# Performance work log

Measured on AMD Instinct MI355X. Metric: run time of the kernel, lower is better.

## Reference

```python
import jax, jax.numpy as jnp
import numpy as np

N_EMBD = 384
N_HEAD = 6
BLOCK_SIZE = 256


def setup_inputs() -> dict:
    key = jax.random.key(0)
    ks = jax.random.split(key, 5)
    B, T = 128, 256
    x = jax.random.normal(ks[0], (B, T, N_EMBD), dtype=jnp.float32)
    # torch nn.Linear weights are (out_features, in_features)
    w_attn = jax.random.normal(ks[1], (3 * N_EMBD, N_EMBD), dtype=jnp.float32) * (1.0 / np.sqrt(N_EMBD))
    b_attn = jax.random.normal(ks[2], (3 * N_EMBD,), dtype=jnp.float32) * 0.02
    w_proj = jax.random.normal(ks[3], (N_EMBD, N_EMBD), dtype=jnp.float32) * (1.0 / np.sqrt(N_EMBD))
    b_proj = jax.random.normal(ks[4], (N_EMBD,), dtype=jnp.float32) * 0.02
    return {"x": x, "w_attn": w_attn, "b_attn": b_attn, "w_proj": w_proj, "b_proj": b_proj}


def reference(x, w_attn, b_attn, w_proj, b_proj):
    B, T, C = x.shape
    hd = C // N_HEAD  # head dim = 64
    qkv = x @ w_attn.T + b_attn                      # [B,T,3C]
    q, k, v = jnp.split(qkv, 3, axis=2)
    # [B,T,C] -> [B,H,T,hd]
    q = q.reshape(B, T, N_HEAD, hd).transpose(0, 2, 1, 3)
    k = k.reshape(B, T, N_HEAD, hd).transpose(0, 2, 1, 3)
    v = v.reshape(B, T, N_HEAD, hd).transpose(0, 2, 1, 3)
    att = jnp.einsum("bhqd,bhkd->bhqk", q, k) * (1.0 / np.sqrt(hd))
    causal = jnp.tril(jnp.ones((T, T), dtype=bool))
    att = jnp.where(causal, att, -jnp.inf)
    att = jax.nn.softmax(att, axis=-1)
    y = jnp.einsum("bhqk,bhkd->bhqd", att, v)        # [B,H,T,hd]
    y = y.transpose(0, 2, 1, 3).reshape(B, T, C)
    return y @ w_proj.T + b_proj
```

## Files before the change

### kernel.cpp

```cpp
#include <hip/hip_runtime.h>
#include <stdint.h>


typedef unsigned short u16;
typedef __attribute__((ext_vector_type(8))) short short8;
typedef __attribute__((ext_vector_type(4))) short short4v;
typedef __attribute__((ext_vector_type(4))) float float4v;

__device__ __forceinline__ u16 f2b(float f){
  union { float f; uint32_t u; } cv; cv.f = f;
  uint32_t u = cv.u;
  u += 0x7FFFu + ((u >> 16) & 1u);
  return (u16)(u >> 16);
}

__device__ __forceinline__ float4v mfma16(short8 a, short8 b, float4v c){
  return __builtin_amdgcn_mfma_f32_16x16x32_bf16(a, b, c, 0, 0, 0);
}

__device__ __forceinline__ void gld16(const void* g, void* l){
  __builtin_amdgcn_global_load_lds((__attribute__((address_space(1))) const void*)g,
                                   (__attribute__((address_space(3))) void*)l, 16, 0, 0);
}

__global__ __launch_bounds__(256) void cvt3(
    const float* __restrict__ a, u16* __restrict__ da, int na,
    const float* __restrict__ b, u16* __restrict__ db, int nb,
    const float* __restrict__ c, u16* __restrict__ dc, int nc)
{
  const int total = na + nb + nc;
  for (int i = blockIdx.x * blockDim.x + threadIdx.x; i < total;
       i += gridDim.x * blockDim.x){
    const float* s; u16* d; int j = i;
    if (j < na)           { s = a; d = da; }
    else if (j < na + nb) { j -= na; s = b; d = db; }
    else                  { j -= na + nb; s = c; d = dc; }
    const float4 v = ((const float4*)s)[j];
    ushort4 o;
    o.x = f2b(v.x); o.y = f2b(v.y); o.z = f2b(v.z); o.w = f2b(v.w);
    ((ushort4*)d)[j] = o;
  }
}

template<bool OUT_BF16>
__global__ __launch_bounds__(256) void gemm_k(
    const u16* __restrict__ A, const u16* __restrict__ B,
    const float* __restrict__ bias, void* __restrict__ Cout,
    const int M, const int N, const int K)
{
  __shared__ u16 Alds[128*32];
  __shared__ u16 Blds[128*32];
  const int tid  = threadIdx.x;
  const int lane = tid & 63;
  const int wave = tid >> 6;
  const int lrow = lane & 15;
  const int g    = lane >> 4;
  const int tm = blockIdx.x * 128;
  const int tn = blockIdx.y * 128;
  const int wm = (wave >> 1) * 64;
  const int wn = (wave & 1) * 64;

  float4v acc[4][4];
  #pragma unroll
  for (int i = 0; i < 4; ++i)
    #pragma unroll
    for (int j = 0; j < 4; ++j) acc[i][j] = (float4v){0.f, 0.f, 0.f, 0.f};

  const int srow = lane >> 2;
  const int scol = (lane & 3) * 8;
  const int nkt = K >> 5;
  for (int kt = 0; kt < nkt; ++kt){
    #pragma unroll
    for (int j2 = 0; j2 < 2; ++j2){
      const int c = wave * 2 + j2;
      const int row = c * 16 + srow;
      gld16(A + (size_t)(tm + row) * K + kt * 32 + scol, &Alds[c * 512]);
      gld16(B + (size_t)(tn + row) * K + kt * 32 + scol, &Blds[c * 512]);
    }
    __syncthreads();
    short8 af[4], bfm[4];
    #pragma unroll
    for (int i = 0; i < 4; ++i){
      af[i]  = *(const short8*)&Alds[(wm + i * 16 + lrow) * 32 + g * 8];
      bfm[i] = *(const short8*)&Blds[(wn + i * 16 + lrow) * 32 + g * 8];
    }
    #pragma unroll
    for (int mi = 0; mi < 4; ++mi)
      #pragma unroll
      for (int ni = 0; ni < 4; ++ni)
        acc[mi][ni] = mfma16(af[mi], bfm[ni], acc[mi][ni]);
    __syncthreads();
  }

  #pragma unroll
  for (int mi = 0; mi < 4; ++mi){
    #pragma unroll
    for (int ni = 0; ni < 4; ++ni){
      const int gcol = tn + wn + ni * 16 + lrow;
      const float bs = bias[gcol];
      #pragma unroll
      for (int r = 0; r < 4; ++r){
        const int grow = tm + wm + mi * 16 + g * 4 + r;
        const float v = acc[mi][ni][r] + bs;
        if (OUT_BF16) ((u16*)Cout)[(size_t)grow * N + gcol] = f2b(v);
        else          ((float*)Cout)[(size_t)grow * N + gcol] = v;
      }
    }
  }
}

__global__ __launch_bounds__(256) void attn_k(
    const u16* __restrict__ qkv, u16* __restrict__ y)
{
  __shared__ u16 Klds[256 * 64];
  __shared__ u16 Vt[64 * 256];
  const int tid  = threadIdx.x;
  const int lane = tid & 63;
  const int wave = tid >> 6;
  const int lrow = lane & 15;
  const int g    = lane >> 4;
  const int bh = blockIdx.x;
  const int b = bh / 6, h = bh % 6;
  const u16* qb = qkv + (size_t)b * 256 * 1152 + h * 64;
  const u16* kb = qb + 384;
  const u16* vb = qb + 768;

  #pragma unroll
  for (int j = 0; j < 8; ++j){
    const int c = wave * 8 + j;
    const int row = c * 8 + (lane >> 3);
    const int col = (((lane & 7) ^ (lane >> 3)) << 3);
    gld16(kb + (size_t)row * 1152 + col, &Klds[c * 512]);
  }
  {
    const int d  = lane;
    const int t0 = wave * 64;
    const int sv = d & 15;
    #pragma unroll
    for (int c4 = 0; c4 < 16; ++c4){
      const size_t base = (size_t)(t0 + c4 * 4) * 1152 + d;
      const u16 e0 = vb[base];
      const u16 e1 = vb[base + 1152];
      const u16 e2 = vb[base + 2304];
      const u16 e3 = vb[base + 3456];
      short4v g4; g4[0] = (short)e0; g4[1] = (short)e1; g4[2] = (short)e2; g4[3] = (short)e3;
      const int pos = (t0 >> 2) + (c4 ^ sv);
      *(short4v*)&Vt[(size_t)d * 256 + (pos << 2)] = g4;
    }
  }
  __syncthreads();

  for (int it = 0; it < 4; ++it){
    const int rb = wave + it * 4;
    const int q0 = rb * 16;
    const u16* qrow = qb + (size_t)(q0 + lrow) * 1152 + g * 8;
    const short8 qf0 = *(const short8*)(qrow);
    const short8 qf1 = *(const short8*)(qrow + 32);

    float4v s[16];
    #pragma unroll
    for (int nt = 0; nt < 16; ++nt){
      if (nt <= rb){
        const int row = nt * 16 + lrow;
        const int sw = lrow & 7;
        const short8 k0 = *(const short8*)&Klds[row * 64 + ((g ^ sw) << 3)];
        const short8 k1 = *(const short8*)&Klds[row * 64 + (((4 + g) ^ sw) << 3)];
        float4v a = (float4v){0.f, 0.f, 0.f, 0.f};
        a = mfma16(k0, qf0, a);
        a = mfma16(k1, qf1, a);
        if (nt == rb){
          #pragma unroll
          for (int r = 0; r < 4; ++r)
            a[r] = (g * 4 + r > lrow) ? -1e30f : a[r];
        }
        s[nt] = a;
      }
    }

    float mx = -1e30f;
    #pragma unroll
    for (int nt = 0; nt < 16; ++nt) if (nt <= rb){
      #pragma unroll
      for (int r = 0; r < 4; ++r) mx = fmaxf(mx, s[nt][r]);
    }
    mx = fmaxf(mx, __shfl_xor(mx, 16));
    mx = fmaxf(mx, __shfl_xor(mx, 32));
    float sum = 0.f;
    #pragma unroll
    for (int nt = 0; nt < 16; ++nt) if (nt <= rb){
      #pragma unroll
      for (int r = 0; r < 4; ++r){
        const float p = exp2f((s[nt][r] - mx) * 0.18033688011112042f);
        s[nt][r] = p;
        sum += p;
      }
    }
    sum += __shfl_xor(sum, 16);
    sum += __shfl_xor(sum, 32);
    const float rs = 1.f / sum;
    #pragma unroll
    for (int nt = 0; nt < 16; ++nt) if (nt <= rb) s[nt] *= rs;

    float4v o0 = (float4v){0,0,0,0}, o1 = (float4v){0,0,0,0};
    float4v o2 = (float4v){0,0,0,0}, o3 = (float4v){0,0,0,0};
    const int svr = lrow;
    #pragma unroll
    for (int kt = 0; kt < 8; ++kt){
      if (2 * kt <= rb){
        short8 pa;
        #pragma unroll
        for (int r = 0; r < 4; ++r) pa[r] = (short)f2b(s[2 * kt][r]);
        if (2 * kt + 1 <= rb){
          #pragma unroll
          for (int r = 0; r < 4; ++r) pa[4 + r] = (short)f2b(s[2 * kt + 1][r]);
        } else {
          #pragma unroll
          for (int r = 0; r < 4; ++r) pa[4 + r] = 0;
        }
        const int plo = ((kt * 8 + g) ^ svr) << 2;
        const int phi = ((kt * 8 + 4 + g) ^ svr) << 2;
        #pragma unroll
        for (int dt = 0; dt < 4; ++dt){
          const u16* vrow = &Vt[(size_t)(dt * 16 + lrow) * 256];
          const short4v vlo = *(const short4v*)&vrow[plo];
          const short4v vhi = *(const short4v*)&vrow[phi];
          const short8 bf = __builtin_shufflevector(vlo, vhi, 0,1,2,3,4,5,6,7);
          if      (dt == 0) o0 = mfma16(pa, bf, o0);
          else if (dt == 1) o1 = mfma16(pa, bf, o1);
          else if (dt == 2) o2 = mfma16(pa, bf, o2);
          else              o3 = mfma16(pa, bf, o3);
        }
      }
    }

    u16* yb = y + (size_t)(b * 256 + q0) * 384 + h * 64;
    #pragma unroll
    for (int r = 0; r < 4; ++r){
      const int q = g * 4 + r;
      yb[(size_t)q * 384 +  0 + lrow] = f2b(o0[r]);
      yb[(size_t)q * 384 + 16 + lrow] = f2b(o1[r]);
      yb[(size_t)q * 384 + 32 + lrow] = f2b(o2[r]);
      yb[(size_t)q * 384 + 48 + lrow] = f2b(o3[r]);
    }
  }
}

extern "C" void kernel_launch(void* const* d_in, const int* in_sizes, int n_in,
                              void* d_out, int out_size, void* d_ws, size_t ws_size,
                              hipStream_t stream)
{
  const float* x      = (const float*)d_in[0];
  const float* w_attn = (const float*)d_in[1];
  const float* b_attn = (const float*)d_in[2];
  const float* w_proj = (const float*)d_in[3];
  const float* b_proj = (const float*)d_in[4];
  float* out = (float*)d_out;

  char* ws = (char*)d_ws;
  u16* xb  = (u16*)(ws);
  u16* wab = (u16*)(ws + 25165824);
  u16* wpb = (u16*)(ws + 26050560);
  u16* qkv = (u16*)(ws + 26345472);
  u16* yb  = (u16*)(ws + 101842944);
  if (ws_size < 127008768) return;

  cvt3<<<2048, 256, 0, stream>>>(x, xb, 3145728,
                                 w_attn, wab, 110592,
                                 w_proj, wpb, 36864);
  gemm_k<true ><<<dim3(256, 9), 256, 0, stream>>>(xb, wab, b_attn, qkv, 32768, 1152, 384);
  attn_k<<<768, 256, 0, stream>>>(qkv, yb);
  gemm_k<false><<<dim3(256, 3), 256, 0, stream>>>(yb, wpb, b_proj, out, 32768, 384, 384);
}
```

Baseline: 127.8 us.

## Double-buffer GEMM LDS tiles, XOR-swizzle LDS layout, and remap blocks per XCD

The GEMM kernel now keeps two LDS buffers and prefetches the next K-slice with global_load_lds while the current one feeds the MFMAs. This removes one barrier per iteration and overlaps loads with compute. The LDS column chunks are XOR-swizzled on both the store and load side to reduce bank conflicts. The launch becomes a 1D grid whose block IDs are remapped so each group of 8 consecutive IDs spreads contiguous M tiles across XCDs, aiming for better L2 reuse. The cost is double the LDS footprint, which may lower occupancy.

New measurement: 125.7 us. Within noise of the previous version (-1.6%).

```diff
diff --git a/kernel.cpp b/kernel.cpp
--- a/kernel.cpp
+++ b/kernel.cpp
@@ -48,15 +48,20 @@
     const float* __restrict__ bias, void* __restrict__ Cout,
     const int M, const int N, const int K)
 {
-  __shared__ u16 Alds[128*32];
-  __shared__ u16 Blds[128*32];
+  __shared__ u16 Alds[2][128*32];
+  __shared__ u16 Blds[2][128*32];
   const int tid  = threadIdx.x;
   const int lane = tid & 63;
   const int wave = tid >> 6;
   const int lrow = lane & 15;
   const int g    = lane >> 4;
-  const int tm = blockIdx.x * 128;
-  const int tn = blockIdx.y * 128;
+
+  const int id    = blockIdx.x;
+  const int local = id >> 3;
+  const int xt = (id & 7) * 32 + (local & 31);
+  const int yt = local >> 5;
+  const int tm = xt * 128;
+  const int tn = yt * 128;
   const int wm = (wave >> 1) * 64;
   const int wn = (wave & 1) * 64;
 
@@ -67,22 +72,30 @@
     for (int j = 0; j < 4; ++j) acc[i][j] = (float4v){0.f, 0.f, 0.f, 0.f};
 
   const int srow = lane >> 2;
-  const int scol = (lane & 3) * 8;
+  const int sg   = ((lane & 3) ^ ((lane >> 3) & 3)) << 3;
+  const int key  = (lrow >> 1) & 3;
+
+  auto STAGE = [&](int kt, int buf){
+    #pragma unroll
+    for (int j = 0; j < 2; ++j){
+      const int c = wave * 2 + j;
+      const int row = c * 16 + srow;
+      gld16(A + (size_t)(tm + row) * K + kt * 32 + sg, &Alds[buf][c * 512]);
+      gld16(B + (size_t)(tn + row) * K + kt * 32 + sg, &Blds[buf][c * 512]);
+    }
+  };
+
   const int nkt = K >> 5;
+  STAGE(0, 0);
+  __syncthreads();
   for (int kt = 0; kt < nkt; ++kt){
-    #pragma unroll
-    for (int j2 = 0; j2 < 2; ++j2){
-      const int c = wave * 2 + j2;
-      const int row = c * 16 + srow;
-      gld16(A + (size_t)(tm + row) * K + kt * 32 + scol, &Alds[c * 512]);
-      gld16(B + (size_t)(tn + row) * K + kt * 32 + scol, &Blds[c * 512]);
-    }
-    __syncthreads();
+    const int buf = kt & 1;
+    if (kt + 1 < nkt) STAGE(kt + 1, buf ^ 1);
     short8 af[4], bfm[4];
     #pragma unroll
     for (int i = 0; i < 4; ++i){
-      af[i]  = *(const short8*)&Alds[(wm + i * 16 + lrow) * 32 + g * 8];
-      bfm[i] = *(const short8*)&Blds[(wn + i * 16 + lrow) * 32 + g * 8];
+      af[i]  = *(const short8*)&Alds[buf][(wm + i * 16 + lrow) * 32 + ((g ^ key) << 3)];
+      bfm[i] = *(const short8*)&Blds[buf][(wn + i * 16 + lrow) * 32 + ((g ^ key) << 3)];
     }
     #pragma unroll
     for (int mi = 0; mi < 4; ++mi)
@@ -162,9 +175,9 @@
     for (int nt = 0; nt < 16; ++nt){
       if (nt <= rb){
         const int row = nt * 16 + lrow;
-        const int sw = lrow & 7;
-        const short8 k0 = *(const short8*)&Klds[row * 64 + ((g ^ sw) << 3)];
-        const short8 k1 = *(const short8*)&Klds[row * 64 + (((4 + g) ^ sw) << 3)];
+        const int swk = lrow & 7;
+        const short8 k0 = *(const short8*)&Klds[row * 64 + ((g ^ swk) << 3)];
+        const short8 k1 = *(const short8*)&Klds[row * 64 + (((4 + g) ^ swk) << 3)];
         float4v a = (float4v){0.f, 0.f, 0.f, 0.f};
         a = mfma16(k0, qf0, a);
         a = mfma16(k1, qf1, a);
@@ -267,7 +280,7 @@
   cvt3<<<2048, 256, 0, stream>>>(x, xb, 3145728,
                                  w_attn, wab, 110592,
                                  w_proj, wpb, 36864);
-  gemm_k<true ><<<dim3(256, 9), 256, 0, stream>>>(xb, wab, b_attn, qkv, 32768, 1152, 384);
+  gemm_k<true ><<<2304, 256, 0, stream>>>(xb, wab, b_attn, qkv, 32768, 1152, 384);
   attn_k<<<768, 256, 0, stream>>>(qkv, yb);
-  gemm_k<false><<<dim3(256, 3), 256, 0, stream>>>(yb, wpb, b_proj, out, 32768, 384, 384);
-}
+  gemm_k<false><<<768, 256, 0, stream>>>(yb, wpb, b_proj, out, 32768, 384, 384);
+}
```
